# Kernel optimization log

Measured on AMD Instinct MI355X. Metric: run time of the kernel, lower is better.

Reference implementation:

```python
import jax, jax.numpy as jnp
import numpy as np

E, H, NH = 512, 2048, 8
HD = E // NH
EPS = 1e-5


def setup_inputs() -> dict:
    key = jax.random.key(0)
    ks = jax.random.split(key, 13)
    s = lambda k, shape, fan_in: jax.random.normal(k, shape, dtype=jnp.float32) * (1.0 / np.sqrt(fan_in))
    return {
        "x": jax.random.normal(ks[0], (1, 4096, E), dtype=jnp.float32),
        "ln_g": jnp.ones((E,), jnp.float32),
        "ln_b": jnp.zeros((E,), jnp.float32),
        "qkv_w": s(ks[1], (3 * E, E), E),
        "qkv_b": jnp.zeros((3 * E,), jnp.float32),
        "proj_w": s(ks[2], (E, E), E),
        "proj_b": jnp.zeros((E,), jnp.float32),
        "fc1_w": s(ks[3], (H, E), E),
        "fc1_b": jnp.zeros((H,), jnp.float32),
        "fc2_w": s(ks[4], (H, H), H),
        "fc2_b": jnp.zeros((H,), jnp.float32),
        "fc3_w": s(ks[5], (E, H), H),
        "fc3_b": jnp.zeros((E,), jnp.float32),
    }


def _layernorm(x, g, b):
    mu = jnp.mean(x, axis=-1, keepdims=True)
    var = jnp.mean(jnp.square(x - mu), axis=-1, keepdims=True)
    return (x - mu) * jax.lax.rsqrt(var + EPS) * g + b


def _attention(h, qkv_w, qkv_b, proj_w, proj_b):
    B, N, _ = h.shape
    qkv = h @ qkv_w.T + qkv_b                      # [B, N, 3E]
    qkv = qkv.reshape(B, N, 3, NH, HD).transpose(2, 0, 3, 1, 4)  # [3, B, NH, N, HD]
    q, k, v = qkv[0], qkv[1], qkv[2]
    scale = HD ** -0.5
    scores = jnp.einsum("bhqd,bhkd->bhqk", q, k) * scale  # full N x N matrix (faithful)
    probs = jax.nn.softmax(scores, axis=-1)
    out = jnp.einsum("bhqk,bhkd->bhqd", probs, v)  # [B, NH, N, HD]
    out = out.transpose(0, 2, 1, 3).reshape(B, N, E)
    return out @ proj_w.T + proj_b


def _mlp(h, fc1_w, fc1_b, fc2_w, fc2_b, fc3_w, fc3_b):
    h = jax.nn.relu(h @ fc1_w.T + fc1_b)
    h = jax.nn.relu(h @ fc2_w.T + fc2_b)
    return h @ fc3_w.T + fc3_b


def reference(x, ln_g, ln_b, qkv_w, qkv_b, proj_w, proj_b,
              fc1_w, fc1_b, fc2_w, fc2_b, fc3_w, fc3_b):
    # Pre-norm block; note the SAME LayerNorm params are used for both sublayers
    x = x + _attention(_layernorm(x, ln_g, ln_b), qkv_w, qkv_b, proj_w, proj_b)
    x = x + _mlp(_layernorm(x, ln_g, ln_b), fc1_w, fc1_b, fc2_w, fc2_b, fc3_w, fc3_b)
    return x
```

## Files before the change

kernel.cpp:

```cpp
#include <hip/hip_runtime.h>
#include <cstdint>
#include <cstddef>

typedef _Float16 f16;
typedef f16 f16x8 __attribute__((ext_vector_type(8)));
typedef float f32x4 __attribute__((ext_vector_type(4)));

#define SLEN 4096
#define EDIM 512
#define TEDIM 1536
#define HDIM 2048
#define NHEAD 8
#define HD 64
#define NSPLIT 4

#define LDS_ASYNC16(gp, lp)                                                      \
  __builtin_amdgcn_global_load_lds(                                              \
      (__attribute__((address_space(1))) void*)(void*)(gp),                      \
      (__attribute__((address_space(3))) void*)(void*)(lp), 16, 0, 0)

struct CvtArgs {
  const float* src[5];
  f16* dst[5];
};
__global__ __launch_bounds__(256) void cvt_all(CvtArgs a) {
  int b = blockIdx.x;
  int seg, off;
  if (b < 384)       { seg = 0; off = b; }
  else if (b < 512)  { seg = 1; off = b - 384; }
  else if (b < 1024) { seg = 2; off = b - 512; }
  else if (b < 3072) { seg = 3; off = b - 1024; }
  else               { seg = 4; off = b - 3072; }
  int i = (off * 256 + threadIdx.x) * 8;
  const float* src = a.src[seg];
  f16* dst = a.dst[seg];
  float4 x = *(const float4*)(src + i);
  float4 y = *(const float4*)(src + i + 4);
  f16x8 o;
  o[0] = (f16)x.x; o[1] = (f16)x.y; o[2] = (f16)x.z; o[3] = (f16)x.w;
  o[4] = (f16)y.x; o[5] = (f16)y.y; o[6] = (f16)y.z; o[7] = (f16)y.w;
  *(f16x8*)(dst + i) = o;
}

__global__ __launch_bounds__(256) void ln_kernel(const float* __restrict__ src,
                                                 const float* __restrict__ g,
                                                 const float* __restrict__ b,
                                                 f16* __restrict__ out) {
  int wave = threadIdx.x >> 6, lane = threadIdx.x & 63;
  int row = blockIdx.x * 4 + wave;
  const float* p = src + (size_t)row * EDIM + lane * 8;
  float v[8];
  float4 a = *(const float4*)p;
  float4 c = *(const float4*)(p + 4);
  v[0] = a.x; v[1] = a.y; v[2] = a.z; v[3] = a.w;
  v[4] = c.x; v[5] = c.y; v[6] = c.z; v[7] = c.w;
  float s = 0.f, s2 = 0.f;
#pragma unroll
  for (int j = 0; j < 8; ++j) { s += v[j]; s2 += v[j] * v[j]; }
#pragma unroll
  for (int m = 1; m < 64; m <<= 1) {
    s += __shfl_xor(s, m, 64);
    s2 += __shfl_xor(s2, m, 64);
  }
  float mu = s * (1.0f / 512.0f);
  float var = s2 * (1.0f / 512.0f) - mu * mu;
  float rs = rsqrtf(var + 1e-5f);
  float4 gg = *(const float4*)(g + lane * 8);
  float4 gh = *(const float4*)(g + lane * 8 + 4);
  float4 bb = *(const float4*)(b + lane * 8);
  float4 bh = *(const float4*)(b + lane * 8 + 4);
  float ga[8] = {gg.x, gg.y, gg.z, gg.w, gh.x, gh.y, gh.z, gh.w};
  float ba[8] = {bb.x, bb.y, bb.z, bb.w, bh.x, bh.y, bh.z, bh.w};
  f16x8 o;
#pragma unroll
  for (int j = 0; j < 8; ++j) o[j] = (f16)((v[j] - mu) * rs * ga[j] + ba[j]);
  *(f16x8*)(out + (size_t)row * EDIM + lane * 8) = o;
}

template <int RELU, int RES, int OUTF32, int BN>
__global__ __launch_bounds__(256) void gemm_bt(const f16* __restrict__ A,
                                               const f16* __restrict__ W,
                                               const float* __restrict__ bias,
                                               const float* __restrict__ res,
                                               void* __restrict__ out,
                                               int M, int Nn, int K) {
  constexpr int MF = (BN == 128) ? 4 : 2;
  __shared__ f16 lA[128 * 64];
  __shared__ f16 lB[BN * 64];
  const int t = threadIdx.x;
  const int wave = t >> 6, lane = t & 63;
  const int wm = (BN == 128) ? (wave >> 1) : wave;
  const int wn = (BN == 128) ? (wave & 1) : 0;
  const int quad = lane >> 4, l15 = lane & 15;
  const int m0 = blockIdx.y * 128, n0 = blockIdx.x * BN;

  f32x4 acc[MF][4] = {};

  const int srow = t >> 3;
  const int scol = (t & 7) * 8;
  const f16* gA = A + (size_t)(m0 + srow) * K + scol;
  const f16* gB = W + (size_t)(n0 + srow) * K + scol;

  for (int k0 = 0; k0 < K; k0 += 64) {
    __syncthreads();
#pragma unroll
    for (int is = 0; is < 4; ++is)
      LDS_ASYNC16(gA + (size_t)(is * 32) * K + k0, lA + is * 2048 + wave * 512);
#pragma unroll
    for (int is = 0; is < BN / 32; ++is)
      LDS_ASYNC16(gB + (size_t)(is * 32) * K + k0, lB + is * 2048 + wave * 512);
    __syncthreads();
#pragma unroll
    for (int ks = 0; ks < 2; ++ks) {
      f16x8 af[MF], bfv[4];
#pragma unroll
      for (int mf = 0; mf < MF; ++mf)
        af[mf] = *(const f16x8*)(lA + (wm * (MF * 16) + mf * 16 + l15) * 64 + ks * 32 + quad * 8);
#pragma unroll
      for (int nf = 0; nf < 4; ++nf)
        bfv[nf] = *(const f16x8*)(lB + (wn * 64 + nf * 16 + l15) * 64 + ks * 32 + quad * 8);
#pragma unroll
      for (int mf = 0; mf < MF; ++mf)
#pragma unroll
        for (int nf = 0; nf < 4; ++nf)
          acc[mf][nf] =
              __builtin_amdgcn_mfma_f32_16x16x32_f16(af[mf], bfv[nf], acc[mf][nf], 0, 0, 0);
    }
  }

  const int mbase = m0 + wm * (MF * 16);
  const int nbase = n0 + wn * 64;
  float bv[4];
#pragma unroll
  for (int nf = 0; nf < 4; ++nf) bv[nf] = bias[nbase + nf * 16 + l15];
#pragma unroll
  for (int mf = 0; mf < MF; ++mf) {
#pragma unroll
    for (int r = 0; r < 4; ++r) {
      size_t m = mbase + mf * 16 + quad * 4 + r;
#pragma unroll
      for (int nf = 0; nf < 4; ++nf) {
        int n = nbase + nf * 16 + l15;
        float v = acc[mf][nf][r] + bv[nf];
        if (RELU) v = v > 0.f ? v : 0.f;
        if (RES) v += res[m * Nn + n];
        if (OUTF32)
          ((float*)out)[m * Nn + n] = v;
        else
          ((f16*)out)[m * Nn + n] = (f16)v;
      }
    }
  }
}

__global__ __launch_bounds__(256) void build_vt(const f16* __restrict__ qkv,
                                                f16* __restrict__ vt) {
  __shared__ f16 tile[64 * 72];
  const int h = blockIdx.x >> 6, nt = blockIdx.x & 63;
  const int t = threadIdx.x;
  const int n0 = nt * 64;
#pragma unroll
  for (int is = 0; is < 2; ++is) {
    int e = is * 2048 + t * 8;
    int nl = e >> 6, d = e & 63;
    f16x8 v = *(const f16x8*)(qkv + (size_t)(n0 + nl) * TEDIM + 1024 + h * 64 + d);
    *(f16x8*)(tile + nl * 72 + d) = v;
  }
  __syncthreads();
  const int d = t >> 2, nc = (t & 3) * 16;
  union { f16 e[16]; f16x8 v[2]; } buf;
#pragma unroll
  for (int j = 0; j < 16; ++j) buf.e[j] = tile[(nc + j) * 72 + d];
  f16* dst = vt + (size_t)h * 64 * SLEN + (size_t)d * SLEN + n0 + nc;
  *(f16x8*)dst = buf.v[0];
  *(f16x8*)(dst + 8) = buf.v[1];
}

__global__ __launch_bounds__(256) void attn_kernel(const f16* __restrict__ qkv,
                                                   const f16* __restrict__ vt,
                                                   f16* __restrict__ Opart,
                                                   float* __restrict__ Lpart) {
  __shared__ f16 lK[64 * 64];
  __shared__ f16 lV[64 * 64];
  __shared__ f16 lP[4][32 * 68];
  const int t = threadIdx.x, wave = t >> 6, lane = t & 63;
  const int quad = lane >> 4, l15 = lane & 15;
  const int split = blockIdx.x & 3;
  const int qb = (blockIdx.x >> 2) & 31;
  const int h = blockIdx.x >> 7;
  const int q0 = qb * 128 + wave * 32;
  const int kv0 = split * (SLEN / NSPLIT);

  f16x8 qf[2][2];
#pragma unroll
  for (int mf = 0; mf < 2; ++mf)
#pragma unroll
    for (int ks = 0; ks < 2; ++ks) {
      f16x8 v = *(const f16x8*)(qkv + (size_t)(q0 + mf * 16 + l15) * TEDIM + h * 64 +
                                ks * 32 + quad * 8);
#pragma unroll
      for (int j = 0; j < 8; ++j) v[j] = v[j] * (f16)0.125f;
      qf[mf][ks] = v;
    }

  f32x4 o[2][4] = {};
  float lsum[2][4] = {};

  const int srow = t >> 3;
  const int scol = (t & 7) * 8;
  const f16* gK = qkv + (size_t)(kv0 + srow) * TEDIM + 512 + h * 64 + scol;
  const f16* gV = vt + (size_t)h * 64 * SLEN + (size_t)srow * SLEN + kv0 + scol;

  for (int kt = 0; kt < (SLEN / NSPLIT) / 64; ++kt) {
    __syncthreads();
#pragma unroll
    for (int is = 0; is < 2; ++is) {
      LDS_ASYNC16(gK + (size_t)(kt * 64 + is * 32) * TEDIM, lK + is * 2048 + wave * 512);
      LDS_ASYNC16(gV + (size_t)(is * 32) * SLEN + kt * 64, lV + is * 2048 + wave * 512);
    }
    __syncthreads();

    f32x4 s[2][4] = {};
#pragma unroll
    for (int ks = 0; ks < 2; ++ks) {
      f16x8 kf[4];
#pragma unroll
      for (int nf = 0; nf < 4; ++nf)
        kf[nf] = *(const f16x8*)(lK + (nf * 16 + l15) * 64 + ks * 32 + quad * 8);
#pragma unroll
      for (int mf = 0; mf < 2; ++mf)
#pragma unroll
        for (int nf = 0; nf < 4; ++nf)
          s[mf][nf] = __builtin_amdgcn_mfma_f32_16x16x32_f16(qf[mf][ks], kf[nf], s[mf][nf], 0, 0, 0);
    }

#pragma unroll
    for (int mf = 0; mf < 2; ++mf)
#pragma unroll
      for (int r = 0; r < 4; ++r) {
        int prow = mf * 16 + quad * 4 + r;
#pragma unroll
        for (int nf = 0; nf < 4; ++nf) {
          float p = __expf(s[mf][nf][r]);
          lsum[mf][r] += p;
          lP[wave][prow * 68 + nf * 16 + l15] = (f16)p;
        }
      }

#pragma unroll
    for (int ks = 0; ks < 2; ++ks) {
      f16x8 pf[2], vf[4];
#pragma unroll
      for (int mf = 0; mf < 2; ++mf)
        pf[mf] = *(const f16x8*)(&lP[wave][(mf * 16 + l15) * 68 + ks * 32 + quad * 8]);
#pragma unroll
      for (int nf = 0; nf < 4; ++nf)
        vf[nf] = *(const f16x8*)(lV + (nf * 16 + l15) * 64 + ks * 32 + quad * 8);
#pragma unroll
      for (int mf = 0; mf < 2; ++mf)
#pragma unroll
        for (int nf = 0; nf < 4; ++nf)
          o[mf][nf] = __builtin_amdgcn_mfma_f32_16x16x32_f16(pf[mf], vf[nf], o[mf][nf], 0, 0, 0);
    }
  }

#pragma unroll
  for (int mf = 0; mf < 2; ++mf)
#pragma unroll
    for (int r = 0; r < 4; ++r) {
      float v = lsum[mf][r];
      v += __shfl_xor(v, 1, 64);
      v += __shfl_xor(v, 2, 64);
      v += __shfl_xor(v, 4, 64);
      v += __shfl_xor(v, 8, 64);
      int row = q0 + mf * 16 + quad * 4 + r;
      if (l15 == 0) Lpart[(size_t)(split * NHEAD + h) * SLEN + row] = v;
      f16* dst = Opart + ((size_t)split * SLEN + row) * EDIM + h * 64;
#pragma unroll
      for (int nf = 0; nf < 4; ++nf) dst[nf * 16 + l15] = (f16)o[mf][nf][r];
    }
}

__global__ __launch_bounds__(256) void attn_combine(const f16* __restrict__ Opart,
                                                    const float* __restrict__ Lpart,
                                                    f16* __restrict__ attn) {
  int idx = (blockIdx.x * 256 + threadIdx.x) * 8;
  int row = idx >> 9;
  int col = idx & 511;
  int h = col >> 6;
  float l = 0.f;
#pragma unroll
  for (int s = 0; s < NSPLIT; ++s) l += Lpart[((size_t)s * NHEAD + h) * SLEN + row];
  float inv = 1.0f / l;
  float acc[8] = {};
#pragma unroll
  for (int s = 0; s < NSPLIT; ++s) {
    f16x8 a = *(const f16x8*)(Opart + ((size_t)s * SLEN + row) * EDIM + col);
#pragma unroll
    for (int j = 0; j < 8; ++j) acc[j] += (float)a[j];
  }
  f16x8 o;
#pragma unroll
  for (int j = 0; j < 8; ++j) o[j] = (f16)(acc[j] * inv);
  *(f16x8*)(attn + (size_t)row * EDIM + col) = o;
}

extern "C" void kernel_launch(void* const* d_in, const int* in_sizes, int n_in,
                              void* d_out, int out_size, void* d_ws, size_t ws_size,
                              hipStream_t stream) {
  const float* x      = (const float*)d_in[0];
  const float* ln_g   = (const float*)d_in[1];
  const float* ln_b   = (const float*)d_in[2];
  const float* qkv_w  = (const float*)d_in[3];
  const float* qkv_b  = (const float*)d_in[4];
  const float* proj_w = (const float*)d_in[5];
  const float* proj_b = (const float*)d_in[6];
  const float* fc1_w  = (const float*)d_in[7];
  const float* fc1_b  = (const float*)d_in[8];
  const float* fc2_w  = (const float*)d_in[9];
  const float* fc2_b  = (const float*)d_in[10];
  const float* fc3_w  = (const float*)d_in[11];
  const float* fc3_b  = (const float*)d_in[12];
  float* out = (float*)d_out;

  char* w = (char*)d_ws;
  f16* wq = (f16*)(w);
  f16* wp = (f16*)(w + (2ull << 20));
  f16* w1 = (f16*)(w + (3ull << 20));
  f16* w2 = (f16*)(w + (5ull << 20));
  f16* w3 = (f16*)(w + (13ull << 20));
  f16* ws_qkv   = (f16*)(w + (15ull << 20));
  f16* ws_vt    = (f16*)(w + (27ull << 20));
  f16* ws_opart = (f16*)(w + (31ull << 20));
  float* ws_lp  = (float*)(w + (47ull << 20));
  f16* ws_attn  = (f16*)(w + (48ull << 20));
  f16* ws_h1    = (f16*)(w + (31ull << 20));
  float* ws_x1  = (float*)(w + (31ull << 20));
  f16* ws_h2    = (f16*)(w + (39ull << 20));
  f16* ws_m1    = (f16*)(w + (15ull << 20));
  f16* ws_m2    = (f16*)(w + (39ull << 20));

  CvtArgs ca;
  ca.src[0] = qkv_w; ca.src[1] = proj_w; ca.src[2] = fc1_w; ca.src[3] = fc2_w; ca.src[4] = fc3_w;
  ca.dst[0] = wq;    ca.dst[1] = wp;     ca.dst[2] = w1;    ca.dst[3] = w2;    ca.dst[4] = w3;
  cvt_all<<<3584, 256, 0, stream>>>(ca);

  ln_kernel<<<SLEN / 4, 256, 0, stream>>>(x, ln_g, ln_b, ws_h1);
  gemm_bt<0, 0, 0, 128><<<dim3(TEDIM / 128, SLEN / 128), 256, 0, stream>>>(
      ws_h1, wq, qkv_b, nullptr, ws_qkv, SLEN, TEDIM, EDIM);
  build_vt<<<NHEAD * (SLEN / 64), 256, 0, stream>>>(ws_qkv, ws_vt);
  attn_kernel<<<NHEAD * (SLEN / 128) * NSPLIT, 256, 0, stream>>>(ws_qkv, ws_vt, ws_opart, ws_lp);
  attn_combine<<<(SLEN * EDIM) / 2048, 256, 0, stream>>>(ws_opart, ws_lp, ws_attn);
  gemm_bt<0, 1, 1, 64><<<dim3(EDIM / 64, SLEN / 128), 256, 0, stream>>>(
      ws_attn, wp, proj_b, x, ws_x1, SLEN, EDIM, EDIM);
  ln_kernel<<<SLEN / 4, 256, 0, stream>>>(ws_x1, ln_g, ln_b, ws_h2);
  gemm_bt<1, 0, 0, 128><<<dim3(HDIM / 128, SLEN / 128), 256, 0, stream>>>(
      ws_h2, w1, fc1_b, nullptr, ws_m1, SLEN, HDIM, EDIM);
  gemm_bt<1, 0, 0, 128><<<dim3(HDIM / 128, SLEN / 128), 256, 0, stream>>>(
      ws_m1, w2, fc2_b, nullptr, ws_m2, SLEN, HDIM, HDIM);
  gemm_bt<0, 1, 1, 64><<<dim3(EDIM / 64, SLEN / 128), 256, 0, stream>>>(
      ws_m2, w3, fc3_b, ws_x1, out, SLEN, EDIM, HDIM);
}
```

Before: 317.0 us.

## Swizzle LDS tiles and keep attention probabilities in registers via transposed S

Adds an XOR swizzle on the 16-byte column chunks of the LDS tiles in both the GEMM and attention kernels, to reduce bank conflicts on the MFMA fragment reads. In attention it computes S transposed (K as the A operand), so each lane's accumulator layout can feed the P·V product directly as the f16x4 operand of a 16x16x16 MFMA. This removes the per-wave LDS round trip for P and simplifies the row-sum reduction. The cost is twice as many smaller MFMA instructions for P·V and more index arithmetic.

Measured after the change: 288.8 us. 1.1x faster.

```diff
diff --git a/kernel.cpp b/kernel.cpp
--- a/kernel.cpp
+++ b/kernel.cpp
@@ -4,6 +4,7 @@
 
 typedef _Float16 f16;
 typedef f16 f16x8 __attribute__((ext_vector_type(8)));
+typedef f16 f16x4 __attribute__((ext_vector_type(4)));
 typedef float f32x4 __attribute__((ext_vector_type(4)));
 
 #define SLEN 4096
@@ -18,6 +19,7 @@
   __builtin_amdgcn_global_load_lds(                                              \
       (__attribute__((address_space(1))) void*)(void*)(gp),                      \
       (__attribute__((address_space(3))) void*)(void*)(lp), 16, 0, 0)
+
 
 struct CvtArgs {
   const float* src[5];
@@ -97,9 +99,10 @@
   f32x4 acc[MF][4] = {};
 
   const int srow = t >> 3;
-  const int scol = (t & 7) * 8;
+  const int scol = (((t & 7) ^ (srow & 7))) * 8;
   const f16* gA = A + (size_t)(m0 + srow) * K + scol;
   const f16* gB = W + (size_t)(n0 + srow) * K + scol;
+  const int sw = (l15 & 7);
 
   for (int k0 = 0; k0 < K; k0 += 64) {
     __syncthreads();
@@ -115,10 +118,12 @@
       f16x8 af[MF], bfv[4];
 #pragma unroll
       for (int mf = 0; mf < MF; ++mf)
-        af[mf] = *(const f16x8*)(lA + (wm * (MF * 16) + mf * 16 + l15) * 64 + ks * 32 + quad * 8);
+        af[mf] = *(const f16x8*)(lA + (wm * (MF * 16) + mf * 16 + l15) * 64 +
+                                 ((ks * 4 + quad) ^ sw) * 8);
 #pragma unroll
       for (int nf = 0; nf < 4; ++nf)
-        bfv[nf] = *(const f16x8*)(lB + (wn * 64 + nf * 16 + l15) * 64 + ks * 32 + quad * 8);
+        bfv[nf] = *(const f16x8*)(lB + (wn * 64 + nf * 16 + l15) * 64 +
+                                  ((ks * 4 + quad) ^ sw) * 8);
 #pragma unroll
       for (int mf = 0; mf < MF; ++mf)
 #pragma unroll
@@ -182,7 +187,6 @@
                                                    float* __restrict__ Lpart) {
   __shared__ f16 lK[64 * 64];
   __shared__ f16 lV[64 * 64];
-  __shared__ f16 lP[4][32 * 68];
   const int t = threadIdx.x, wave = t >> 6, lane = t & 63;
   const int quad = lane >> 4, l15 = lane & 15;
   const int split = blockIdx.x & 3;
@@ -190,6 +194,7 @@
   const int h = blockIdx.x >> 7;
   const int q0 = qb * 128 + wave * 32;
   const int kv0 = split * (SLEN / NSPLIT);
+  const int sw = (l15 & 7);
 
   f16x8 qf[2][2];
 #pragma unroll
@@ -204,10 +209,10 @@
     }
 
   f32x4 o[2][4] = {};
-  float lsum[2][4] = {};
+  float lsum[2] = {0.f, 0.f};
 
   const int srow = t >> 3;
-  const int scol = (t & 7) * 8;
+  const int scol = ((t & 7) ^ (srow & 7)) * 8;
   const f16* gK = qkv + (size_t)(kv0 + srow) * TEDIM + 512 + h * 64 + scol;
   const f16* gV = vt + (size_t)h * 64 * SLEN + (size_t)srow * SLEN + kv0 + scol;
 
@@ -220,61 +225,60 @@
     }
     __syncthreads();
 
-    f32x4 s[2][4] = {};
+    f32x4 st[4][2] = {};
 #pragma unroll
     for (int ks = 0; ks < 2; ++ks) {
-      f16x8 kf[4];
+      f16x8 kfr[4];
+#pragma unroll
+      for (int cf = 0; cf < 4; ++cf)
+        kfr[cf] = *(const f16x8*)(lK + (cf * 16 + l15) * 64 + ((ks * 4 + quad) ^ sw) * 8);
+#pragma unroll
+      for (int cf = 0; cf < 4; ++cf)
+#pragma unroll
+        for (int mf = 0; mf < 2; ++mf)
+          st[cf][mf] =
+              __builtin_amdgcn_mfma_f32_16x16x32_f16(kfr[cf], qf[mf][ks], st[cf][mf], 0, 0, 0);
+    }
+
+    f16x4 pf[4][2];
+#pragma unroll
+    for (int cf = 0; cf < 4; ++cf)
+#pragma unroll
+      for (int mf = 0; mf < 2; ++mf)
+#pragma unroll
+        for (int r = 0; r < 4; ++r) {
+          float p = __expf(st[cf][mf][r]);
+          lsum[mf] += p;
+          pf[cf][mf][r] = (f16)p;
+        }
+
+#pragma unroll
+    for (int cf = 0; cf < 4; ++cf) {
+      f16x4 vfr[4];
 #pragma unroll
       for (int nf = 0; nf < 4; ++nf)
-        kf[nf] = *(const f16x8*)(lK + (nf * 16 + l15) * 64 + ks * 32 + quad * 8);
+        vfr[nf] = *(const f16x4*)(lV + (nf * 16 + l15) * 64 +
+                                  (((cf * 2 + (quad >> 1)) ^ sw) * 8) + (quad & 1) * 4);
 #pragma unroll
       for (int mf = 0; mf < 2; ++mf)
 #pragma unroll
         for (int nf = 0; nf < 4; ++nf)
-          s[mf][nf] = __builtin_amdgcn_mfma_f32_16x16x32_f16(qf[mf][ks], kf[nf], s[mf][nf], 0, 0, 0);
-    }
-
-#pragma unroll
-    for (int mf = 0; mf < 2; ++mf)
-#pragma unroll
-      for (int r = 0; r < 4; ++r) {
-        int prow = mf * 16 + quad * 4 + r;
-#pragma unroll
-        for (int nf = 0; nf < 4; ++nf) {
-          float p = __expf(s[mf][nf][r]);
-          lsum[mf][r] += p;
-          lP[wave][prow * 68 + nf * 16 + l15] = (f16)p;
-        }
-      }
-
-#pragma unroll
-    for (int ks = 0; ks < 2; ++ks) {
-      f16x8 pf[2], vf[4];
-#pragma unroll
-      for (int mf = 0; mf < 2; ++mf)
-        pf[mf] = *(const f16x8*)(&lP[wave][(mf * 16 + l15) * 68 + ks * 32 + quad * 8]);
-#pragma unroll
-      for (int nf = 0; nf < 4; ++nf)
-        vf[nf] = *(const f16x8*)(lV + (nf * 16 + l15) * 64 + ks * 32 + quad * 8);
-#pragma unroll
-      for (int mf = 0; mf < 2; ++mf)
-#pragma unroll
-        for (int nf = 0; nf < 4; ++nf)
-          o[mf][nf] = __builtin_amdgcn_mfma_f32_16x16x32_f16(pf[mf], vf[nf], o[mf][nf], 0, 0, 0);
-    }
-  }
-
+          o[mf][nf] = __builtin_amdgcn_mfma_f32_16x16x16f16(pf[cf][mf], vfr[nf], o[mf][nf], 0, 0, 0);
+    }
+  }
+
+#pragma unroll
+  for (int mf = 0; mf < 2; ++mf) {
+    float v = lsum[mf];
+    v += __shfl_xor(v, 16, 64);
+    v += __shfl_xor(v, 32, 64);
+    if (quad == 0) Lpart[(size_t)(split * NHEAD + h) * SLEN + q0 + mf * 16 + l15] = v;
+  }
 #pragma unroll
   for (int mf = 0; mf < 2; ++mf)
 #pragma unroll
     for (int r = 0; r < 4; ++r) {
-      float v = lsum[mf][r];
-      v += __shfl_xor(v, 1, 64);
-      v += __shfl_xor(v, 2, 64);
-      v += __shfl_xor(v, 4, 64);
-      v += __shfl_xor(v, 8, 64);
       int row = q0 + mf * 16 + quad * 4 + r;
-      if (l15 == 0) Lpart[(size_t)(split * NHEAD + h) * SLEN + row] = v;
       f16* dst = Opart + ((size_t)split * SLEN + row) * EDIM + h * 64;
 #pragma unroll
       for (int nf = 0; nf < 4; ++nf) dst[nf * 16 + l15] = (f16)o[mf][nf][r];
```
